# Kernel tuning notes

Measured on AMD Instinct MI355X. Metric: run time of the kernel, lower is better.

The kernel has to match this reference:

```python
import jax, jax.numpy as jnp
import numpy as np

BLOCK_LEN = 128
NUM_HEADS = 16


def setup_inputs() -> dict:
    key = jax.random.key(0)
    k0, k1, k2 = jax.random.split(key, 3)
    D = 1024
    x = jax.random.normal(k0, (2, 8192, D), dtype=jnp.float32)
    Wqkv = jax.random.normal(k1, (D, 3 * D), dtype=jnp.float32) * 0.02
    bqkv = jnp.zeros((3 * D,), dtype=jnp.float32)
    Wout = jax.random.normal(k2, (D, D), dtype=jnp.float32) * 0.02
    bout = jnp.zeros((D,), dtype=jnp.float32)
    return {"x": x, "Wqkv": Wqkv, "bqkv": bqkv, "Wout": Wout, "bout": bout}


def reference(x, Wqkv, bqkv, Wout, bout):
    B, S, D = x.shape
    H = NUM_HEADS
    BL = BLOCK_LEN
    NB = S // BL            # number of blocks (rows)
    HD = D // H             # head dim (qkv_ratio=1.0 -> qkv_dim_total == D)

    qkv = x @ Wqkv + bqkv                                   # [B, S, 3D]
    qkv = qkv.reshape(B, NB, BL, 3, H, HD)
    q = qkv[:, :, :, 0]                                     # [B, NB, BL, H, HD]
    k = qkv[:, :, :, 1]
    v = qkv[:, :, :, 2]

    # 'column' attention: attend across blocks at the same within-block position.
    # permute to [B, BL(pos p), H, NB(block n), HD]
    qc = jnp.transpose(q, (0, 2, 3, 1, 4))
    kc = jnp.transpose(k, (0, 2, 3, 1, 4))
    vc = jnp.transpose(v, (0, 2, 3, 1, 4))

    scale = 1.0 / jnp.sqrt(jnp.asarray(HD, dtype=x.dtype))
    scores = jnp.einsum('bphnd,bphmd->bphnm', qc, kc) * scale   # [B,BL,H,NB,NB]
    causal = jnp.tril(jnp.ones((NB, NB), dtype=bool))
    scores = jnp.where(causal, scores, jnp.asarray(-1e9, dtype=scores.dtype))
    w = jax.nn.softmax(scores, axis=-1)
    o = jnp.einsum('bphnm,bphmd->bphnd', w, vc)                 # [B,BL,H,NB,HD]

    # back to [B, NB, BL, H*HD] -> [B, S, D]
    o = jnp.transpose(o, (0, 3, 1, 2, 4)).reshape(B, S, D)
    return o @ Wout + bout
```

## Files before the change

kernel.cpp:

```cpp
#include <hip/hip_runtime.h>
#include <stdint.h>

typedef unsigned short u16;
typedef __attribute__((ext_vector_type(8))) short s16x8;
typedef __attribute__((ext_vector_type(4))) float f32x4;

__device__ __forceinline__ f32x4 mfma16x16(s16x8 a, s16x8 b, f32x4 c) {
    return __builtin_amdgcn_mfma_f32_16x16x32_bf16(a, b, c, 0, 0, 0);
}

__device__ __forceinline__ u16 f2bf(float f) {
    union { float f; unsigned u; } c; c.f = f;
    unsigned u = c.u;
    return (u16)((u + 0x7FFFu + ((u >> 16) & 1u)) >> 16);
}

__device__ __forceinline__ void gload16(const void* g, void* l) {
    auto gp = (const __attribute__((address_space(1))) unsigned int*)(g);
    auto lp = (__attribute__((address_space(3))) unsigned int*)(l);
    __builtin_amdgcn_global_load_lds(gp, lp, 16, 0, 0);
}

__device__ __forceinline__ void wave_sync() {
    __builtin_amdgcn_sched_barrier(0);
    asm volatile("s_waitcnt vmcnt(0) lgkmcnt(0)" ::: "memory");
    __builtin_amdgcn_sched_barrier(0);
    __builtin_amdgcn_s_barrier();
    __builtin_amdgcn_sched_barrier(0);
}

__global__ __launch_bounds__(256) void convert_x(
    const float* __restrict__ src, u16* __restrict__ dst, long n)
{
    const long stride = (long)gridDim.x * 256 * 8;
    for (long i = ((long)blockIdx.x * 256 + threadIdx.x) * 8; i < n; i += stride) {
        const float4 a = *(const float4*)(src + i);
        const float4 b = *(const float4*)(src + i + 4);
        u16 o[8] = { f2bf(a.x), f2bf(a.y), f2bf(a.z), f2bf(a.w),
                     f2bf(b.x), f2bf(b.y), f2bf(b.z), f2bf(b.w) };
        *(s16x8*)(dst + i) = *(const s16x8*)o;
    }
}

__global__ __launch_bounds__(256) void fill_sentinel(float* __restrict__ o, long n)
{
    const long stride = (long)gridDim.x * 256;
    for (long i = (long)blockIdx.x * 256 + threadIdx.x; i < n; i += stride)
        o[i] = 1.0f;
}

__global__ __launch_bounds__(256) void transpose_f32_bf16(
    const float* __restrict__ in, u16* __restrict__ out, int R, int C)
{
    __shared__ u16 t[32][33];
    const int c0 = blockIdx.x * 32, r0 = blockIdx.y * 32;
    const int tx = threadIdx.x & 31, ty = threadIdx.x >> 5;
#pragma unroll
    for (int i = 0; i < 32; i += 8)
        t[ty + i][tx] = f2bf(in[(long)(r0 + ty + i) * C + c0 + tx]);
    __syncthreads();
#pragma unroll
    for (int i = 0; i < 32; i += 8)
        out[(long)(c0 + ty + i) * R + r0 + tx] = t[tx][ty + i];
}

template <int FP32OUT, int NT, int NBN>
__global__ __launch_bounds__(256, 2) void gemm128x256(
    const u16* __restrict__ A, const u16* __restrict__ BT,
    const float* __restrict__ bias, void* __restrict__ Cout,
    int N, int K)
{
    __shared__ u16 As[2][8192];

    const int tid  = threadIdx.x;
    const int lane = tid & 63;
    const int wid  = tid >> 6;
    const int rr   = lane & 15, g = lane >> 4;

    const int nwg = gridDim.x;
    const int gsw = ((int)blockIdx.x & 7) * (nwg >> 3) + ((int)blockIdx.x >> 3);
    const long m0 = (long)(gsw / NBN) * 128;
    const long n0 = (long)(gsw % NBN) * 256;

    const u16* pA[4];
    int ldst[4];
#pragma unroll
    for (int p = 0; p < 4; ++p) {
        const int r = (wid * 4 + p) * 8 + (lane >> 3);
        const int c = (lane & 7) ^ (r & 7);
        pA[p]   = A + (m0 + r) * (long)K + c * 8;
        ldst[p] = (wid * 4 + p) * 1024;
    }
    const u16* pB[4];
#pragma unroll
    for (int n = 0; n < 4; ++n)
        pB[n] = BT + (n0 + wid * 64 + n * 16 + rr) * (long)K + g * 8;

    int aoff[2];
#pragma unroll
    for (int kk = 0; kk < 2; ++kk)
        aoff[kk] = rr * 128 + ((kk * 64 + g * 16) ^ ((rr & 7) << 4));

#define STA(tt) { char* d_ = (char*)As[(tt) & 1];                             \
    _Pragma("unroll") for (int p_ = 0; p_ < 4; ++p_)                          \
        gload16(pA[p_] + (long)(tt) * 64, d_ + ldst[p_]); }
#define LDB(dst, tt, kk) { _Pragma("unroll") for (int n_ = 0; n_ < 4; ++n_)   \
    dst[n_] = *(const s16x8*)(pB[n_] + (long)(tt) * 64 + (kk) * 32); }
#define SB() __builtin_amdgcn_sched_barrier(0)

    f32x4 acc[8][4] = {};
    s16x8 B0a[4], B1a[4], B0b[4], B1b[4];

    STA(0);
    LDB(B0a, 0, 0);
    asm volatile("s_waitcnt vmcnt(4)" ::: "memory");
    SB(); __builtin_amdgcn_s_barrier(); SB();

#define SUBCLUSTER(bufi, kk, mb, Bf)                                          \
    { s16x8 fA[4];                                                            \
      _Pragma("unroll") for (int m_ = 0; m_ < 4; ++m_)                        \
          fA[m_] = *(const s16x8*)((const char*)As[bufi] +                    \
                    ((mb) + m_) * 2048 + aoff[kk]);                           \
      SB();                                                                   \
      __builtin_amdgcn_s_setprio(1);                                          \
      _Pragma("unroll") for (int m_ = 0; m_ < 4; ++m_)                        \
      _Pragma("unroll") for (int n_ = 0; n_ < 4; ++n_)                        \
          acc[(mb) + m_][n_] = mfma16x16(fA[m_], Bf[n_], acc[(mb) + m_][n_]); \
      __builtin_amdgcn_s_setprio(0);                                          \
      SB(); }

#define TILE(t_, Bc0, Bc1, Bn0)                                               \
    {                                                                         \
        if ((t_) + 1 < NT) STA((t_) + 1);                                     \
        LDB(Bc1, (t_), 1);                                                    \
        SUBCLUSTER((t_) & 1, 0, 0, Bc0)                                       \
        SUBCLUSTER((t_) & 1, 0, 4, Bc0)                                       \
        if ((t_) + 1 < NT) LDB(Bn0, (t_) + 1, 0);                             \
        SUBCLUSTER((t_) & 1, 1, 0, Bc1)                                       \
        SUBCLUSTER((t_) & 1, 1, 4, Bc1)                                       \
        if ((t_) < NT - 1) {                                                  \
            asm volatile("s_waitcnt vmcnt(4)" ::: "memory");                  \
            SB(); __builtin_amdgcn_s_barrier(); SB();                         \
        }                                                                     \
    }

    for (int i = 0; i < NT / 2; ++i) {
        TILE(2 * i,     B0a, B1a, B0b)
        TILE(2 * i + 1, B0b, B1b, B0a)
    }
#undef TILE
#undef SUBCLUSTER
#undef STA
#undef LDB
#undef SB

    float bv[4];
#pragma unroll
    for (int n = 0; n < 4; ++n)
        bv[n] = bias[n0 + wid * 64 + n * 16 + rr];
#pragma unroll
    for (int m = 0; m < 8; ++m) {
        const long rb = m0 + m * 16 + g * 4;
#pragma unroll
        for (int r = 0; r < 4; ++r) {
            const long rowoff = (rb + r) * N + n0 + wid * 64 + rr;
#pragma unroll
            for (int n = 0; n < 4; ++n) {
                const float v = acc[m][n][r] + bv[n];
                if (FP32OUT) ((float*)Cout)[rowoff + n * 16] = v;
                else         ((u16*)Cout)[rowoff + n * 16] = f2bf(v);
            }
        }
    }
}

__global__ __launch_bounds__(64) void attn_blocks(
    const u16* __restrict__ qkv, u16* __restrict__ o)
{
    __shared__ u16 Vlds[64 * 64];
    __shared__ u16 Plds[64 * 72];
    const int bid = blockIdx.x;
    const int b = bid >> 11;
    const int h = (bid >> 7) & 15;
    const int p = bid & 127;
    const int lane = threadIdx.x;
    const int rr = lane & 15, g = lane >> 4;
    const long NSTR = 128L * 3072;
    const long base = ((long)b * 8192 + p) * 3072 + h * 64;

    {
        const int vrow = lane >> 3;
        const int vchunk = (lane & 7) ^ (vrow & 7);
#pragma unroll
        for (int q = 0; q < 8; ++q)
            gload16(qkv + base + (long)(q * 8 + vrow) * NSTR + 2048 + vchunk * 8,
                    (char*)Vlds + q * 1024);
    }

    s16x8 kf[4][2], qf[4][2];
#pragma unroll
    for (int t = 0; t < 4; ++t)
#pragma unroll
        for (int ks = 0; ks < 2; ++ks) {
            const long roff = base + (long)(t * 16 + rr) * NSTR + ks * 32 + g * 8;
            kf[t][ks] = *(const s16x8*)(qkv + roff + 1024);
            qf[t][ks] = *(const s16x8*)(qkv + roff);
        }

    f32x4 T[4][4] = {};
#pragma unroll
    for (int ks = 0; ks < 2; ++ks)
#pragma unroll
        for (int i = 0; i < 4; ++i)
#pragma unroll
            for (int jn = 0; jn < 4; ++jn)
                T[i][jn] = mfma16x16(kf[i][ks], qf[jn][ks], T[i][jn]);

    const float scale = 0.125f;
#pragma unroll
    for (int jn = 0; jn < 4; ++jn) {
        const int n = jn * 16 + rr;
        float pv[16];
        float mx = -3e38f;
#pragma unroll
        for (int i = 0; i < 4; ++i)
#pragma unroll
            for (int r = 0; r < 4; ++r) {
                const int m = i * 16 + g * 4 + r;
                const float s = (m <= n) ? T[i][jn][r] * scale : -3e38f;
                pv[i * 4 + r] = s;
                mx = fmaxf(mx, s);
            }
        mx = fmaxf(mx, __shfl_xor(mx, 16));
        mx = fmaxf(mx, __shfl_xor(mx, 32));
        float sum = 0.f;
#pragma unroll
        for (int t = 0; t < 16; ++t) {
            const float e = (pv[t] > -1e30f) ? __expf(pv[t] - mx) : 0.f;
            pv[t] = e;
            sum += e;
        }
        sum += __shfl_xor(sum, 16);
        sum += __shfl_xor(sum, 32);
        const float inv = 1.f / sum;
#pragma unroll
        for (int i = 0; i < 4; ++i)
#pragma unroll
            for (int rp = 0; rp < 2; ++rp) {
                const int m = i * 16 + g * 4 + rp * 2;
                const unsigned lo = f2bf(pv[i * 4 + rp * 2] * inv);
                const unsigned hi = f2bf(pv[i * 4 + rp * 2 + 1] * inv);
                *(unsigned*)((char*)Plds + n * 144 + m * 2) = lo | (hi << 16);
            }
    }

    wave_sync();

    f32x4 O[4][4] = {};
#pragma unroll
    for (int ks = 0; ks < 2; ++ks) {
        s16x8 pa[4];
#pragma unroll
        for (int in = 0; in < 4; ++in)
            pa[in] = *(const s16x8*)((const char*)Plds +
                      (in * 16 + rr) * 144 + ks * 64 + g * 16);
#pragma unroll
        for (int jd = 0; jd < 4; ++jd) {
            s16x8 vb;
#pragma unroll
            for (int j = 0; j < 8; ++j) {
                const int k = ks * 32 + g * 8 + j;
                const int byte = (k * 128 + (jd * 16 + rr) * 2) ^ ((k & 7) << 4);
                vb[j] = *(const short*)((const char*)Vlds + byte);
            }
#pragma unroll
            for (int in = 0; in < 4; ++in)
                O[in][jd] = mfma16x16(pa[in], vb, O[in][jd]);
        }
    }

    const long obase = ((long)b * 8192 + p) * 1024 + h * 64;
#pragma unroll
    for (int in = 0; in < 4; ++in)
#pragma unroll
        for (int r = 0; r < 4; ++r) {
            const long n = in * 16 + g * 4 + r;
#pragma unroll
            for (int jd = 0; jd < 4; ++jd) {
                const long d = jd * 16 + rr;
                o[obase + n * (128L * 1024) + d] = f2bf(O[in][jd][r]);
            }
        }
}

extern "C" void kernel_launch(void* const* d_in, const int* in_sizes, int n_in,
                              void* d_out, int out_size, void* d_ws, size_t ws_size,
                              hipStream_t stream) {
    const float* x    = (const float*)d_in[0];
    const float* Wqkv = (const float*)d_in[1];
    const float* bq   = (const float*)d_in[2];
    const float* Wout = (const float*)d_in[3];
    const float* bo   = (const float*)d_in[4];

    char* ws = (char*)d_ws;
    u16* xb    = (u16*)(ws);
    u16* qkv   = (u16*)(ws +  33554432L);
    u16* ob    = (u16*)(ws + 134217728L);
    u16* WqkvT = (u16*)(ws + 167772160L);
    u16* WoutT = (u16*)(ws + 174063616L);
    const size_t NEEDED = 176160768UL;

    if (ws_size < NEEDED) {
        fill_sentinel<<<2048, 256, 0, stream>>>((float*)d_out, (long)out_size);
        return;
    }

    convert_x<<<2048, 256, 0, stream>>>(x, xb, 16777216L);
    transpose_f32_bf16<<<dim3(96, 32), 256, 0, stream>>>(Wqkv, WqkvT, 1024, 3072);
    transpose_f32_bf16<<<dim3(32, 32), 256, 0, stream>>>(Wout, WoutT, 1024, 1024);

    gemm128x256<0, 16, 12><<<1536, 256, 0, stream>>>(xb, WqkvT, bq, qkv,
                                                     3072, 1024);

    attn_blocks<<<4096, 64, 0, stream>>>(qkv, ob);

    gemm128x256<1, 16, 4><<<512, 256, 0, stream>>>(ob, WoutT, bo, d_out,
                                                   1024, 1024);
}
```

Measured before the change: 215.9 us.

## Switch GEMMs to 256x256 tiles with 8 waves and LDS-staged A and B

Replaces the 128x256 GEMM, which streamed B fragments straight from global memory per wave, with a 256x256 tile computed by 512 threads (2x4 waves). Both A and B are now staged into 128KB of dynamic LDS through double-buffered half-K stages with swizzled layout. The aim is to raise arithmetic intensity and cut redundant global B traffic. In exchange, the large LDS footprint limits occupancy to about one workgroup per CU, and the grid shrinks to 768 and 256 workgroups, which may underfill the machine for the output GEMM.

```diff
diff --git a/kernel.cpp b/kernel.cpp
--- a/kernel.cpp
+++ b/kernel.cpp
@@ -65,105 +65,104 @@
 }
 
 template <int FP32OUT, int NT, int NBN>
-__global__ __launch_bounds__(256, 2) void gemm128x256(
+__global__ __launch_bounds__(512, 2) void gemm256(
     const u16* __restrict__ A, const u16* __restrict__ BT,
     const float* __restrict__ bias, void* __restrict__ Cout,
     int N, int K)
 {
-    __shared__ u16 As[2][8192];
+    extern __shared__ char smem[];
+    char* const As = smem;
+    char* const Bs = smem + 65536;
 
     const int tid  = threadIdx.x;
     const int lane = tid & 63;
     const int wid  = tid >> 6;
     const int rr   = lane & 15, g = lane >> 4;
+    const int wr   = wid >> 2;
+    const int wc   = wid & 3;
 
     const int nwg = gridDim.x;
     const int gsw = ((int)blockIdx.x & 7) * (nwg >> 3) + ((int)blockIdx.x >> 3);
-    const long m0 = (long)(gsw / NBN) * 128;
+    const long m0 = (long)(gsw / NBN) * 256;
     const long n0 = (long)(gsw % NBN) * 256;
 
-    const u16* pA[4];
-    int ldst[4];
-#pragma unroll
-    for (int p = 0; p < 4; ++p) {
-        const int r = (wid * 4 + p) * 8 + (lane >> 3);
-        const int c = (lane & 7) ^ (r & 7);
-        pA[p]   = A + (m0 + r) * (long)K + c * 8;
-        ldst[p] = (wid * 4 + p) * 1024;
-    }
-    const u16* pB[4];
-#pragma unroll
-    for (int n = 0; n < 4; ++n)
-        pB[n] = BT + (n0 + wid * 64 + n * 16 + rr) * (long)K + g * 8;
-
-    int aoff[2];
-#pragma unroll
-    for (int kk = 0; kk < 2; ++kk)
-        aoff[kk] = rr * 128 + ((kk * 64 + g * 16) ^ ((rr & 7) << 4));
-
-#define STA(tt) { char* d_ = (char*)As[(tt) & 1];                             \
-    _Pragma("unroll") for (int p_ = 0; p_ < 4; ++p_)                          \
-        gload16(pA[p_] + (long)(tt) * 64, d_ + ldst[p_]); }
-#define LDB(dst, tt, kk) { _Pragma("unroll") for (int n_ = 0; n_ < 4; ++n_)   \
-    dst[n_] = *(const s16x8*)(pB[n_] + (long)(tt) * 64 + (kk) * 32); }
+    const int cl = (tid & 3) ^ ((tid >> 3) & 3);
+    const u16* pA0 = A  + (m0 + (tid >> 2)) * (long)K + cl * 8;
+    const u16* pA1 = pA0 + 128 * (long)K;
+    const u16* pB0 = BT + (n0 + (tid >> 2)) * (long)K + cl * 8;
+    const u16* pB1 = pB0 + 128 * (long)K;
+    const int sdst = wid * 1024;
+
+    const int xg   = (g ^ ((rr >> 1) & 3)) << 4;
+    const int arow = (wr * 128 + rr) * 64 + xg;
+    const int brow = (wc * 64  + rr) * 64 + xg;
+
+#define STA(tt, h) { const long c_ = (long)(tt) * 64 + (h) * 32;              \
+        char* d_ = As + (((tt) & 1) * 2 + (h)) * 16384 + sdst;                \
+        gload16(pA0 + c_, d_); gload16(pA1 + c_, d_ + 8192); }
+#define STB(tt, h) { const long c_ = (long)(tt) * 64 + (h) * 32;              \
+        char* d_ = Bs + (((tt) & 1) * 2 + (h)) * 16384 + sdst;                \
+        gload16(pB0 + c_, d_); gload16(pB1 + c_, d_ + 8192); }
 #define SB() __builtin_amdgcn_sched_barrier(0)
+#define RD(Bf, Af, half, bufsel)                                              \
+    { _Pragma("unroll") for (int n_ = 0; n_ < 4; ++n_)                        \
+          Bf[n_] = *(const s16x8*)(Bs + (bufsel) + (half) + brow + n_ * 1024);\
+      _Pragma("unroll") for (int m_ = 0; m_ < 8; ++m_)                        \
+          Af[m_] = *(const s16x8*)(As + (bufsel) + (half) + arow + m_ * 1024);}
+#define MM(Af, Bf)                                                            \
+    { SB(); __builtin_amdgcn_s_setprio(1);                                    \
+      _Pragma("unroll") for (int m_ = 0; m_ < 8; ++m_)                        \
+      _Pragma("unroll") for (int n_ = 0; n_ < 4; ++n_)                        \
+          acc[m_][n_] = mfma16x16(Af[m_], Bf[n_], acc[m_][n_]);               \
+      __builtin_amdgcn_s_setprio(0); SB(); }
 
     f32x4 acc[8][4] = {};
-    s16x8 B0a[4], B1a[4], B0b[4], B1b[4];
-
-    STA(0);
-    LDB(B0a, 0, 0);
+    s16x8 B0[4], A0[8], B1[4], A1[8];
+
+    STA(0, 0); STB(0, 0); STA(0, 1); STB(0, 1); STA(1, 0); STB(1, 0);
     asm volatile("s_waitcnt vmcnt(4)" ::: "memory");
     SB(); __builtin_amdgcn_s_barrier(); SB();
-
-#define SUBCLUSTER(bufi, kk, mb, Bf)                                          \
-    { s16x8 fA[4];                                                            \
-      _Pragma("unroll") for (int m_ = 0; m_ < 4; ++m_)                        \
-          fA[m_] = *(const s16x8*)((const char*)As[bufi] +                    \
-                    ((mb) + m_) * 2048 + aoff[kk]);                           \
-      SB();                                                                   \
-      __builtin_amdgcn_s_setprio(1);                                          \
-      _Pragma("unroll") for (int m_ = 0; m_ < 4; ++m_)                        \
-      _Pragma("unroll") for (int n_ = 0; n_ < 4; ++n_)                        \
-          acc[(mb) + m_][n_] = mfma16x16(fA[m_], Bf[n_], acc[(mb) + m_][n_]); \
-      __builtin_amdgcn_s_setprio(0);                                          \
-      SB(); }
-
-#define TILE(t_, Bc0, Bc1, Bn0)                                               \
-    {                                                                         \
-        if ((t_) + 1 < NT) STA((t_) + 1);                                     \
-        LDB(Bc1, (t_), 1);                                                    \
-        SUBCLUSTER((t_) & 1, 0, 0, Bc0)                                       \
-        SUBCLUSTER((t_) & 1, 0, 4, Bc0)                                       \
-        if ((t_) + 1 < NT) LDB(Bn0, (t_) + 1, 0);                             \
-        SUBCLUSTER((t_) & 1, 1, 0, Bc1)                                       \
-        SUBCLUSTER((t_) & 1, 1, 4, Bc1)                                       \
-        if ((t_) < NT - 1) {                                                  \
-            asm volatile("s_waitcnt vmcnt(4)" ::: "memory");                  \
-            SB(); __builtin_amdgcn_s_barrier(); SB();                         \
-        }                                                                     \
-    }
-
-    for (int i = 0; i < NT / 2; ++i) {
-        TILE(2 * i,     B0a, B1a, B0b)
-        TILE(2 * i + 1, B0b, B1b, B0a)
-    }
-#undef TILE
-#undef SUBCLUSTER
+    RD(B0, A0, 0, 0);
+
+    for (int t = 0; t < NT; ++t) {
+        const int ab = (t & 1) * 32768;
+        const int nb = ((t + 1) & 1) * 32768;
+
+        if (t > 0) {
+            if (t == NT - 1) { asm volatile("s_waitcnt vmcnt(0)" ::: "memory"); }
+            else             { asm volatile("s_waitcnt vmcnt(4)" ::: "memory"); }
+            SB(); __builtin_amdgcn_s_barrier(); SB();
+        }
+        RD(B1, A1, 16384, ab);
+        SB();
+        if (t + 1 < NT) { STA(t + 1, 1); STB(t + 1, 1); }
+        MM(A0, B0);
+
+        if (t < NT - 1) {
+            asm volatile("s_waitcnt vmcnt(4)" ::: "memory");
+            SB(); __builtin_amdgcn_s_barrier(); SB();
+            RD(B0, A0, 0, nb);
+            SB();
+            if (t + 2 < NT) { STA(t + 2, 0); STB(t + 2, 0); }
+        }
+        MM(A1, B1);
+    }
 #undef STA
-#undef LDB
+#undef STB
 #undef SB
+#undef RD
+#undef MM
 
     float bv[4];
 #pragma unroll
     for (int n = 0; n < 4; ++n)
-        bv[n] = bias[n0 + wid * 64 + n * 16 + rr];
+        bv[n] = bias[n0 + wc * 64 + n * 16 + rr];
 #pragma unroll
     for (int m = 0; m < 8; ++m) {
-        const long rb = m0 + m * 16 + g * 4;
+        const long rb = m0 + wr * 128 + m * 16 + g * 4;
 #pragma unroll
         for (int r = 0; r < 4; ++r) {
-            const long rowoff = (rb + r) * N + n0 + wid * 64 + rr;
+            const long rowoff = (rb + r) * N + n0 + wc * 64 + rr;
 #pragma unroll
             for (int n = 0; n < 4; ++n) {
                 const float v = acc[m][n][r] + bv[n];
@@ -315,15 +314,20 @@
         return;
     }
 
+    (void)hipFuncSetAttribute(reinterpret_cast<const void*>(&gemm256<0, 16, 12>),
+                              hipFuncAttributeMaxDynamicSharedMemorySize, 131072);
+    (void)hipFuncSetAttribute(reinterpret_cast<const void*>(&gemm256<1, 16, 4>),
+                              hipFuncAttributeMaxDynamicSharedMemorySize, 131072);
+
     convert_x<<<2048, 256, 0, stream>>>(x, xb, 16777216L);
     transpose_f32_bf16<<<dim3(96, 32), 256, 0, stream>>>(Wqkv, WqkvT, 1024, 3072);
     transpose_f32_bf16<<<dim3(32, 32), 256, 0, stream>>>(Wout, WoutT, 1024, 1024);
 
-    gemm128x256<0, 16, 12><<<1536, 256, 0, stream>>>(xb, WqkvT, bq, qkv,
+    gemm256<0, 16, 12><<<768, 512, 131072, stream>>>(xb, WqkvT, bq, qkv,
                                                      3072, 1024);
 
     attn_blocks<<<4096, 64, 0, stream>>>(qkv, ob);
 
-    gemm128x256<1, 16, 4><<<512, 256, 0, stream>>>(ob, WoutT, bo, d_out,
-                                                   1024, 1024);
-}
+    gemm256<1, 16, 4><<<256, 512, 131072, stream>>>(ob, WoutT, bo, d_out,
+                                                    1024, 1024);
+}
```

Measured after the change: 210.8 us. 2.4% less time.
